# Performance work log

Hardware: AMD Instinct MI355X
Metric: run time of the kernel (lower is better)

Reference implementation:

```python
import jax, jax.numpy as jnp
import numpy as np

G = 512            # voxel grid extent per axis
B = 2              # batches
N_PER_BATCH = 20000
EPS = 1e-5
SLOPE = 0.01       # LeakyReLU default negative_slope
OFFS = [(dx, dy, dz) for dx in (-1, 0, 1) for dy in (-1, 0, 1) for dz in (-1, 0, 1)]


def _keys(coords, stride):
    # coords: [N,4] int32 (batch,x,y,z), multiples of stride -> unique int32 key
    Gs = G // stride
    c = coords[:, 1:] // stride
    return ((coords[:, 0] * Gs + c[:, 0]) * Gs + c[:, 1]) * Gs + c[:, 2]


def _sorted_keys(in_coords, in_stride):
    keys = _keys(in_coords, in_stride)
    perm = jnp.argsort(keys)
    return keys[perm], perm


def _query(ks, perm, out_coords, off, in_stride):
    # hash-free kernel-map lookup: binary search of neighbor key in sorted keys
    q = out_coords[:, 1:] + jnp.array(off, jnp.int32) * in_stride
    valid = jnp.all((q >= 0) & (q < G), axis=1)
    qc = jnp.clip(q, 0, G - 1) // in_stride
    Gs = G // in_stride
    qk = ((out_coords[:, 0] * Gs + qc[:, 0]) * Gs + qc[:, 1]) * Gs + qc[:, 2]
    pos = jnp.clip(jnp.searchsorted(ks, qk), 0, ks.shape[0] - 1)
    hit = valid & (ks[pos] == qk)
    return jnp.where(hit, perm[pos], 0), hit


def sparse_conv(feats, in_coords, out_coords, W, in_stride):
    # gather-GEMM-scatter sparse conv, kernel 3^3, W: [27, Cin, Cout]
    ks, perm = _sorted_keys(in_coords, in_stride)
    out = jnp.zeros((out_coords.shape[0], W.shape[-1]), feats.dtype)
    for k, off in enumerate(OFFS):
        idx, hit = _query(ks, perm, out_coords, off, in_stride)
        f = jnp.where(hit[:, None], feats[idx], jnp.zeros((), feats.dtype))
        out = out + f @ W[k]
    return out


def sparse_maxpool(feats, in_coords, out_coords, in_stride):
    ks, perm = _sorted_keys(in_coords, in_stride)
    NEG = jnp.asarray(-3.0e38, feats.dtype)
    out = jnp.full((out_coords.shape[0], feats.shape[1]), NEG, feats.dtype)
    for off in OFFS:
        idx, hit = _query(ks, perm, out_coords, off, in_stride)
        out = jnp.maximum(out, jnp.where(hit[:, None], feats[idx], NEG))
    return out


def slice_to_field(level_feats, level_coords, field_coords, stride):
    # TensorField.slice: map coarse sparse features back to every field point
    ks, perm = _sorted_keys(level_coords, stride)
    qk = _keys(field_coords, stride)
    pos = jnp.clip(jnp.searchsorted(ks, qk), 0, ks.shape[0] - 1)
    return level_feats[perm[pos]]


def bn_lrelu(x, gamma, beta):
    # MinkowskiBatchNorm (training-mode batch stats) + LeakyReLU
    mu = x.mean(0)
    var = ((x - mu) ** 2).mean(0)
    y = (x - mu) * jax.lax.rsqrt(var + EPS) * gamma + beta
    return jnp.where(y >= 0, y, SLOPE * y)


def setup_inputs() -> dict:
    rng = np.random.default_rng(0)
    coords_np = []
    for b in range(B):
        lin = np.unique(rng.integers(0, G ** 3, size=2 * N_PER_BATCH, dtype=np.int64))
        rng.shuffle(lin)
        lin = lin[:N_PER_BATCH]
        x, r = lin // (G * G), lin % (G * G)
        coords_np.append(np.stack([np.full(N_PER_BATCH, b, np.int64), x, r // G, r % G], 1))
    coords_np = np.concatenate(coords_np, 0)

    def level(s):
        q = coords_np.copy()
        q[:, 1:] = (q[:, 1:] // s) * s
        key = ((q[:, 0] * G + q[:, 1]) * G + q[:, 2]) * G + q[:, 3]
        uk = np.unique(key)
        b, r = uk // G ** 3, uk % G ** 3
        return np.stack([b, r // (G * G), (r // G) % G, r % G], 1).astype(np.int32)

    levels = {('c%d' % s): jnp.asarray(level(s)) for s in (2, 4, 8, 16, 32, 64, 128)}
    ks = jax.random.split(jax.random.key(0), 9)

    def conv_w(k, cin, cout):
        return jax.random.normal(k, (27, cin, cout), jnp.float32) * np.float32(np.sqrt(2.0 / (27 * cin)))

    inp = dict(
        feats=jax.random.normal(ks[0], (coords_np.shape[0], 1), jnp.float32),
        coords=jnp.asarray(coords_np.astype(np.int32)),
        w_mlp=jax.random.normal(ks[1], (1, 32), jnp.float32),
        gm=jnp.ones(32, jnp.float32), bm=jnp.zeros(32, jnp.float32),
        W1=conv_w(ks[2], 32, 48), g1=jnp.ones(48, jnp.float32), b1=jnp.zeros(48, jnp.float32),
        W2=conv_w(ks[3], 48, 64), g2=jnp.ones(64, jnp.float32), b2=jnp.zeros(64, jnp.float32),
        W3=conv_w(ks[4], 64, 96), g3=jnp.ones(96, jnp.float32), b3=jnp.zeros(96, jnp.float32),
        W4=conv_w(ks[5], 96, 128), g4=jnp.ones(128, jnp.float32), b4=jnp.zeros(128, jnp.float32),
        W5a=conv_w(ks[6], 336, 256), g5a=jnp.ones(256, jnp.float32), b5a=jnp.zeros(256, jnp.float32),
        W5b=conv_w(ks[7], 256, 512), g5b=jnp.ones(512, jnp.float32), b5b=jnp.zeros(512, jnp.float32),
        W5c=conv_w(ks[8], 512, 1024), g5c=jnp.ones(1024, jnp.float32), b5c=jnp.zeros(1024, jnp.float32),
    )
    inp.update(levels)
    return inp


def reference(feats, coords, c2, c4, c8, c16, c32, c64, c128, w_mlp, gm, bm,
              W1, g1, b1, W2, g2, b2, W3, g3, b3, W4, g4, b4,
              W5a, g5a, b5a, W5b, g5b, b5b, W5c, g5c, b5c):
    # mlp1 on the tensor field (coords are unique, so field == sparse tensor)
    x = bn_lrelu(feats @ w_mlp, gm, bm)                            # [N,32]
    y = bn_lrelu(sparse_conv(x, coords, coords, W1, 1), g1, b1)    # stride 1, 48
    y1 = sparse_maxpool(y, coords, c2, 1)                          # stride 2
    y = bn_lrelu(sparse_conv(y1, c2, c4, W2, 2), g2, b2)           # stride 4, 64
    y2 = sparse_maxpool(y, c4, c8, 4)                              # stride 8
    y = bn_lrelu(sparse_conv(y2, c8, c16, W3, 8), g3, b3)          # stride 16, 96
    y3 = sparse_maxpool(y, c16, c32, 16)                           # stride 32
    y = bn_lrelu(sparse_conv(y3, c32, c64, W4, 32), g4, b4)        # stride 64, 128
    y4 = sparse_maxpool(y, c64, c128, 64)                          # stride 128
    x1 = slice_to_field(y1, c2, coords, 2)
    x2 = slice_to_field(y2, c8, coords, 8)
    x3 = slice_to_field(y3, c32, coords, 32)
    x4 = slice_to_field(y4, c128, coords, 128)
    xc = jnp.concatenate([x1, x2, x3, x4], axis=1)                 # [N,336]
    y = bn_lrelu(sparse_conv(xc, coords, c2, W5a, 1), g5a, b5a)    # stride 2, 256
    y = bn_lrelu(sparse_conv(y, c2, c4, W5b, 2), g5b, b5b)         # stride 4, 512
    y = bn_lrelu(sparse_conv(y, c4, c8, W5c, 4), g5c, b5c)         # stride 8, 1024
    return y
```

## Files before the change

kernel.cpp:

```cpp
#include <hip/hip_runtime.h>
#include <cstdint>
#include <cstddef>

#define GDIM 512

typedef __attribute__((ext_vector_type(8))) short short8;
typedef __attribute__((ext_vector_type(4))) float f32x4;
typedef __attribute__((ext_vector_type(4))) unsigned short ushort4v;

__device__ __forceinline__ short f2bf(float f) {
  unsigned u = __float_as_uint(f);
  u = u + 0x7fffu + ((u >> 16) & 1u);
  return (short)(u >> 16);
}

__device__ __forceinline__ int hash_lookup(int key, const int* __restrict__ keys,
                                           const int* __restrict__ vals, unsigned capmask) {
  unsigned slot = ((unsigned)key * 2654435761u) & capmask;
  while (true) {
    int kk = keys[slot];
    if (kk == key) return vals[slot];
    if (kk == -1) return -1;
    slot = (slot + 1) & capmask;
  }
}

__global__ void k_build_table(const int* __restrict__ coords, int n, int sh, int Gs,
                              int* __restrict__ keys, int* __restrict__ vals, unsigned capmask) {
  int i = blockIdx.x * blockDim.x + threadIdx.x;
  if (i >= n) return;
  int b = coords[4 * i];
  int key = ((b * Gs + (coords[4 * i + 1] >> sh)) * Gs + (coords[4 * i + 2] >> sh)) * Gs +
            (coords[4 * i + 3] >> sh);
  unsigned slot = ((unsigned)key * 2654435761u) & capmask;
  while (true) {
    int prev = atomicCAS(&keys[slot], -1, key);
    if (prev == -1) { vals[slot] = i; return; }
    slot = (slot + 1) & capmask;
  }
}

__global__ void k_query_idx_t(const int* __restrict__ oc, int m, int sh, int Gs,
                              const int* __restrict__ keys, const int* __restrict__ vals,
                              unsigned capmask, int* __restrict__ idxT) {
  int k = blockIdx.y;
  int o = blockIdx.x * blockDim.x + threadIdx.x;
  if (o >= m) return;
  int stride = 1 << sh;
  int dx = k / 9 - 1, dy = (k / 3) % 3 - 1, dz = k % 3 - 1;
  int4 c = *(const int4*)(oc + 4 * o);
  int qx = c.y + dx * stride;
  int qy = c.z + dy * stride;
  int qz = c.w + dz * stride;
  int res = -1;
  if ((unsigned)qx < GDIM && (unsigned)qy < GDIM && (unsigned)qz < GDIM) {
    int key = ((c.x * Gs + (qx >> sh)) * Gs + (qy >> sh)) * Gs + (qz >> sh);
    res = hash_lookup(key, keys, vals, capmask);
  }
  idxT[(size_t)k * m + o] = res;
}

__global__ void k_make_pairs(const int* __restrict__ idxT, int m,
                             int* __restrict__ po_o, int* __restrict__ pi_o,
                             int* __restrict__ po_r, int* __restrict__ pi_r,
                             int* __restrict__ cnts, int mcap) {
  int o = blockIdx.x * blockDim.x + threadIdx.x;
  bool act = o < m;
  int lane = threadIdx.x & 63;
  bool owned = false;
  for (int k = 0; k < 27; ++k) {
    int i = act ? idxT[(size_t)k * m + o] : -1;
    bool hit = i >= 0;
    bool isown = hit && !owned;
    if (isown) owned = true;
    bool isrest = hit && !isown;
    unsigned long long bo = __ballot(isown);
    if (bo) {
      int ldr = __ffsll((unsigned long long)bo) - 1;
      int base = 0;
      if (lane == ldr) base = atomicAdd(&cnts[k], __popcll(bo));
      base = __shfl(base, ldr);
      if (isown) {
        int p = base + __popcll(bo & ((1ull << lane) - 1ull));
        po_o[k * mcap + p] = o;
        pi_o[k * mcap + p] = i;
      }
    }
    unsigned long long br = __ballot(isrest);
    if (br) {
      int ldr = __ffsll((unsigned long long)br) - 1;
      int base = 0;
      if (lane == ldr) base = atomicAdd(&cnts[27 + k], __popcll(br));
      base = __shfl(base, ldr);
      if (isrest) {
        int p = base + __popcll(br & ((1ull << lane) - 1ull));
        po_r[k * mcap + p] = o;
        pi_r[k * mcap + p] = i;
      }
    }
  }
}

__global__ void k_plan(const int* __restrict__ cnts, int* __restrict__ plan) {
  if (threadIdx.x == 0) {
    int acc = 0;
    for (int k = 0; k < 27; ++k) { plan[k] = acc; acc += (cnts[k] + 63) >> 6; }
    plan[27] = acc;
    acc = 0;
    for (int k = 0; k < 27; ++k) { plan[28 + k] = acc; acc += (cnts[27 + k] + 63) >> 6; }
    plan[55] = acc;
  }
}

template<bool OWNER>
__global__ __launch_bounds__(256) void k_conv_mfma(
    const unsigned short* __restrict__ Fb,
    const short* __restrict__ Wt,
    float* __restrict__ out,
    const int* __restrict__ plo, const int* __restrict__ pli,
    const int* __restrict__ counts, const int* __restrict__ plan,
    int cin, int cin_pad, int cout, int mcap) {
  __shared__ int pshared[28];
  __shared__ short Alds[64 * 136];
  __shared__ short Blds[2][128 * 40];
  __shared__ int rows_out[64];
  __shared__ int rows_in[64];

  int tid = threadIdx.x;
  if (tid < 28) pshared[tid] = plan[tid];
  __syncthreads();
  int NB = pshared[27];

  int n0 = blockIdx.y << 7;
  int wave = tid >> 6, lane = tid & 63;
  int wm = (wave & 1) * 32, wn = (wave >> 1) * 64;
  int lm = lane & 15, quad = lane >> 4;
  int bn0 = (tid) >> 2, bk0 = (tid & 3) << 3;
  int bn1 = (tid + 256) >> 2, bk1 = ((tid + 256) & 3) << 3;

  for (int v = blockIdx.x; v < NB; v += gridDim.x) {
    int k = 0;
    #pragma unroll
    for (int kk = 1; kk < 27; ++kk) k += (v >= pshared[kk]);
    int cnt = counts[k];
    int p0 = (v - pshared[k]) << 6;
    int np = min(64, cnt - p0);

    __syncthreads();
    if (tid < 64) {
      rows_out[tid] = (tid < np) ? plo[k * mcap + p0 + tid] : -1;
      rows_in [tid] = (tid < np) ? pli[k * mcap + p0 + tid] : -1;
    }
    const short* Wk = Wt + (size_t)k * cout * cin;
    f32x4 acc[2][4] = {};

    for (int ks = 0; ks < cin_pad; ks += 128) {
      int kslab = min(128, cin_pad - ks);
      int aStride = kslab + 8;
      __syncthreads();
      int clog = kslab == 128 ? 4 : (kslab == 64 ? 3 : 2);
      for (int u = tid; u < (64 << clog); u += 256) {
        int r = u >> clog;
        int kc = (u - (r << clog)) << 3;
        int gk = ks + kc;
        int irow = rows_in[r];
        short8 v8 = {0, 0, 0, 0, 0, 0, 0, 0};
        if (irow >= 0 && gk < cin)
          v8 = *(const short8*)((const short*)Fb + (size_t)irow * cin + gk);
        *(short8*)(Alds + r * aStride + kc) = v8;
      }
      int nsl = kslab >> 5;
      short8 br0 = {0, 0, 0, 0, 0, 0, 0, 0}, br1 = br0;
      {
        int gn = n0 + bn0, gk = ks + bk0;
        if (gn < cout && gk < cin) br0 = *(const short8*)(Wk + (size_t)gn * cin + gk);
        gn = n0 + bn1; gk = ks + bk1;
        if (gn < cout && gk < cin) br1 = *(const short8*)(Wk + (size_t)gn * cin + gk);
      }
      for (int j = 0; j < nsl; ++j) {
        __syncthreads();
        *(short8*)(&Blds[j & 1][bn0 * 40 + bk0]) = br0;
        *(short8*)(&Blds[j & 1][bn1 * 40 + bk1]) = br1;
        if (j + 1 < nsl) {
          int gkbase = ks + (j + 1) * 32;
          short8 z = {0, 0, 0, 0, 0, 0, 0, 0};
          br0 = z; br1 = z;
          int gn = n0 + bn0, gk = gkbase + bk0;
          if (gn < cout && gk < cin) br0 = *(const short8*)(Wk + (size_t)gn * cin + gk);
          gn = n0 + bn1; gk = gkbase + bk1;
          if (gn < cout && gk < cin) br1 = *(const short8*)(Wk + (size_t)gn * cin + gk);
        }
        __syncthreads();
        int ka = j * 32 + quad * 8;
        short8 a0 = *(const short8*)(Alds + (wm + lm) * aStride + ka);
        short8 a1 = *(const short8*)(Alds + (wm + 16 + lm) * aStride + ka);
        #pragma unroll
        for (int nt = 0; nt < 4; ++nt) {
          short8 b = *(const short8*)(&Blds[j & 1][(wn + nt * 16 + lm) * 40 + quad * 8]);
          acc[0][nt] = __builtin_amdgcn_mfma_f32_16x16x32_bf16(a0, b, acc[0][nt], 0, 0, 0);
          acc[1][nt] = __builtin_amdgcn_mfma_f32_16x16x32_bf16(a1, b, acc[1][nt], 0, 0, 0);
        }
      }
    }
    #pragma unroll
    for (int mt = 0; mt < 2; ++mt)
      #pragma unroll
      for (int nt = 0; nt < 4; ++nt)
        #pragma unroll
        for (int r = 0; r < 4; ++r) {
          int row = wm + mt * 16 + quad * 4 + r;
          int col = n0 + wn + nt * 16 + lm;
          if (row < np && col < cout) {
            if (OWNER)
              out[(size_t)rows_out[row] * cout + col] = acc[mt][nt][r];
            else
              atomicAdd(&out[(size_t)rows_out[row] * cout + col], acc[mt][nt][r]);
          }
        }
  }
}

__global__ void k_convert_w(const float* __restrict__ W, short* __restrict__ Wt,
                            int cin, int cout) {
  __shared__ float tile[32][33];
  int k = blockIdx.z;
  int n0 = blockIdx.x * 32, c0 = blockIdx.y * 32;
  int tx = threadIdx.x & 31, ty = threadIdx.x >> 5;
  const float* Wk = W + (size_t)k * cin * cout;
  for (int i = ty; i < 32; i += 8) {
    int c = c0 + i, n = n0 + tx;
    tile[i][tx] = (c < cin && n < cout) ? Wk[(size_t)c * cout + n] : 0.f;
  }
  __syncthreads();
  short* Wtk = Wt + (size_t)k * cout * cin;
  for (int i = ty; i < 32; i += 8) {
    int n = n0 + i, c = c0 + tx;
    if (n < cout && c < cin) Wtk[(size_t)n * cin + c] = f2bf(tile[tx][i]);
  }
}

__global__ void k_query_idx(const int* __restrict__ oc, int m, int sh, int Gs,
                            const int* __restrict__ keys, const int* __restrict__ vals,
                            unsigned capmask, int* __restrict__ idx) {
  int t = blockIdx.x * blockDim.x + threadIdx.x;
  if (t >= m * 27) return;
  int o = t / 27, k = t - o * 27;
  int stride = 1 << sh;
  int dx = k / 9 - 1, dy = (k / 3) % 3 - 1, dz = k % 3 - 1;
  int b  = oc[4 * o];
  int qx = oc[4 * o + 1] + dx * stride;
  int qy = oc[4 * o + 2] + dy * stride;
  int qz = oc[4 * o + 3] + dz * stride;
  int res = -1;
  if ((unsigned)qx < GDIM && (unsigned)qy < GDIM && (unsigned)qz < GDIM) {
    int key = ((b * Gs + (qx >> sh)) * Gs + (qy >> sh)) * Gs + (qz >> sh);
    res = hash_lookup(key, keys, vals, capmask);
  }
  idx[t] = res;
}

__global__ void k_maxpool_bn(const float* __restrict__ F, unsigned short* __restrict__ out,
                             const int* __restrict__ idx, int m, int C,
                             const float* __restrict__ ab) {
  long long t = (long long)blockIdx.x * blockDim.x + threadIdx.x;
  if (t >= (long long)m * C) return;
  int o = (int)(t / C), c = (int)(t - (long long)o * C);
  float a = ab[c], b = ab[C + c];
  float best = -3e38f;
  #pragma unroll 1
  for (int k = 0; k < 27; ++k) {
    int i = idx[o * 27 + k];
    if (i >= 0) {
      float y = a * F[(size_t)i * C + c] + b;
      y = fmaxf(y, 0.01f * y);
      best = fmaxf(best, y);
    }
  }
  out[t] = (unsigned short)f2bf(best);
}

__global__ void k_slice_idx(const int* __restrict__ coords, int n, int sh, int Gs,
                            const int* __restrict__ keys, const int* __restrict__ vals,
                            unsigned capmask, int* __restrict__ sidx) {
  int i = blockIdx.x * blockDim.x + threadIdx.x;
  if (i >= n) return;
  int b = coords[4 * i];
  int key = ((b * Gs + (coords[4 * i + 1] >> sh)) * Gs + (coords[4 * i + 2] >> sh)) * Gs +
            (coords[4 * i + 3] >> sh);
  int v = hash_lookup(key, keys, vals, capmask);
  sidx[i] = (v < 0) ? 0 : v;
}

__global__ void k_gather_cols16(const unsigned short* __restrict__ src, int C,
                                const int* __restrict__ sidx,
                                unsigned short* __restrict__ dst, int dstC, int colOff, int n) {
  long long t = (long long)blockIdx.x * blockDim.x + threadIdx.x;
  if (t >= (long long)n * C) return;
  int o = (int)(t / C), c = (int)(t - (long long)o * C);
  dst[(size_t)o * dstC + colOff + c] = src[(size_t)sidx[o] * C + c];
}

__global__ void k_mlp(const float* __restrict__ feats, const float* __restrict__ w,
                      float* __restrict__ x, int n) {
  int t = blockIdx.x * blockDim.x + threadIdx.x;
  if (t >= n * 32) return;
  x[t] = feats[t >> 5] * w[t & 31];
}

__global__ void k_bn_stats(const float* __restrict__ x, int m, int C,
                           float* __restrict__ sums) {
  __shared__ float ls[2][256];
  int tid = threadIdx.x;
  int RL = (C >= 256) ? 1 : (256 / C);
  int c, rl;
  bool active;
  if (C >= 256) { c = blockIdx.y * 256 + tid; rl = 0; active = true; }
  else { c = tid % C; rl = tid / C; active = (tid < RL * C); }
  float s = 0.f, s2 = 0.f;
  if (active) {
    int step = gridDim.x * RL;
    for (int r = blockIdx.x * RL + rl; r < m; r += step) {
      float v = x[(size_t)r * C + c];
      s += v; s2 += v * v;
    }
  }
  if (RL == 1) {
    atomicAdd(&sums[c], s);
    atomicAdd(&sums[C + c], s2);
  } else {
    ls[0][tid] = s; ls[1][tid] = s2;
    __syncthreads();
    if (tid < C) {
      for (int j = 1; j < RL; ++j) { s += ls[0][c + j * C]; s2 += ls[1][c + j * C]; }
      atomicAdd(&sums[c], s);
      atomicAdd(&sums[C + c], s2);
    }
  }
}

__global__ void k_bn_finalize(const float* __restrict__ sums, const float* __restrict__ gamma,
                              const float* __restrict__ beta, int C, float inv_m,
                              float* __restrict__ ab) {
  for (int c = threadIdx.x; c < C; c += 256) {
    float mu  = sums[c] * inv_m;
    float var = sums[C + c] * inv_m - mu * mu;
    float a = rsqrtf(var + 1e-5f) * gamma[c];
    ab[c] = a;
    ab[C + c] = beta[c] - mu * a;
  }
}

__global__ void k_bn_bf16(const float* __restrict__ x, unsigned short* __restrict__ xb,
                          long long total4, int C, const float* __restrict__ ab) {
  long long t = (long long)blockIdx.x * blockDim.x + threadIdx.x;
  if (t >= total4) return;
  long long e = t * 4;
  int c = (int)(e % C);
  float4 v = *(const float4*)(x + e);
  ushort4v o;
  float y0 = ab[c] * v.x + ab[C + c];         o.x = (unsigned short)f2bf(fmaxf(y0, 0.01f * y0));
  float y1 = ab[c + 1] * v.y + ab[C + c + 1]; o.y = (unsigned short)f2bf(fmaxf(y1, 0.01f * y1));
  float y2 = ab[c + 2] * v.z + ab[C + c + 2]; o.z = (unsigned short)f2bf(fmaxf(y2, 0.01f * y2));
  float y3 = ab[c + 3] * v.w + ab[C + c + 3]; o.w = (unsigned short)f2bf(fmaxf(y3, 0.01f * y3));
  *(ushort4v*)(xb + e) = o;
}

__global__ void k_bn_apply(float* __restrict__ x, long long total4, int C,
                           const float* __restrict__ ab) {
  long long t = (long long)blockIdx.x * blockDim.x + threadIdx.x;
  if (t >= total4) return;
  long long e = t * 4;
  int c = (int)(e % C);
  float4 v = *(const float4*)(x + e);
  float y0 = ab[c] * v.x + ab[C + c];         v.x = fmaxf(y0, 0.01f * y0);
  float y1 = ab[c + 1] * v.y + ab[C + c + 1]; v.y = fmaxf(y1, 0.01f * y1);
  float y2 = ab[c + 2] * v.z + ab[C + c + 2]; v.z = fmaxf(y2, 0.01f * y2);
  float y3 = ab[c + 3] * v.w + ab[C + c + 3]; v.w = fmaxf(y3, 0.01f * y3);
  *(float4*)(x + e) = v;
}

static inline int cdiv(int a, int b) { return (a + b - 1) / b; }

extern "C" void kernel_launch(void* const* d_in, const int* in_sizes, int n_in,
                              void* d_out, int out_size, void* d_ws, size_t ws_size,
                              hipStream_t stream) {
  (void)n_in; (void)out_size; (void)ws_size;
  const float* feats  = (const float*)d_in[0];
  const int*   coords = (const int*)d_in[1];
  const float* w_mlp = (const float*)d_in[2];
  const float* gm  = (const float*)d_in[3];  const float* bm  = (const float*)d_in[4];
  const float* W1  = (const float*)d_in[5];  const float* g1  = (const float*)d_in[6];  const float* b1  = (const float*)d_in[7];
  const float* W2  = (const float*)d_in[8];  const float* g2  = (const float*)d_in[9];  const float* b2  = (const float*)d_in[10];
  const float* W3  = (const float*)d_in[11]; const float* g3  = (const float*)d_in[12]; const float* b3  = (const float*)d_in[13];
  const float* W4  = (const float*)d_in[14]; const float* g4  = (const float*)d_in[15]; const float* b4  = (const float*)d_in[16];
  const float* W5a = (const float*)d_in[17]; const float* g5a = (const float*)d_in[18]; const float* b5a = (const float*)d_in[19];
  const float* W5b = (const float*)d_in[20]; const float* g5b = (const float*)d_in[21]; const float* b5b = (const float*)d_in[22];
  const float* W5c = (const float*)d_in[23]; const float* g5c = (const float*)d_in[24]; const float* b5c = (const float*)d_in[25];
  const int*   lvl[7];
  for (int i = 0; i < 7; ++i) lvl[i] = (const int*)d_in[26 + i];

  const int N = in_sizes[0];
  int nl[7];
  for (int i = 0; i < 7; ++i) nl[i] = in_sizes[26 + i] / 4;
  const int n2 = nl[0], n4 = nl[1], n8 = nl[2], n16 = nl[3], n32 = nl[4], n64 = nl[5], n128 = nl[6];

  char* ws = (char*)d_ws;
  size_t off = 0;
  auto alloc = [&](size_t bytes) -> char* {
    off = (off + 255) & ~(size_t)255;
    char* p = ws + off;
    off += bytes;
    return p;
  };

  struct Tab { int* keys; int* vals; unsigned mask; int sh; int Gs; int n; const int* src; };
  Tab tab[8];
  const int* tsrc[8] = {coords, lvl[0], lvl[1], lvl[2], lvl[3], lvl[4], lvl[5], lvl[6]};
  int tn[8] = {N, n2, n4, n8, n16, n32, n64, n128};
  for (int i = 0; i < 8; ++i) {
    int cap = 64;
    while (cap < 2 * tn[i]) cap <<= 1;
    tab[i].keys = (int*)alloc((size_t)cap * 4);
    tab[i].vals = (int*)alloc((size_t)cap * 4);
    tab[i].mask = (unsigned)(cap - 1);
    tab[i].sh = i;
    tab[i].Gs = GDIM >> i;
    tab[i].n = tn[i];
    tab[i].src = tsrc[i];
  }

  int* pout   = (int*)alloc((size_t)27 * N * 4);
  int* pin    = (int*)alloc((size_t)27 * N * 4);
  int* pout_r = (int*)alloc((size_t)27 * N * 4);
  int* pin_r  = (int*)alloc((size_t)27 * N * 4);
  int* counts = (int*)alloc(256);
  int* plan   = (int*)alloc(256);
  int* idxbuf = (int*)alloc((size_t)27 * N * 4);
  int* sidx[4];
  for (int i = 0; i < 4; ++i) sidx[i] = (int*)alloc((size_t)N * 4);
  float* bnsum = (float*)alloc(2 * 1024 * 4);
  float* abuf  = (float*)alloc(2 * 1024 * 4);

  auto mxz = [](size_t a, size_t b) { return a > b ? a : b; };
  size_t szA = mxz(mxz((size_t)N * 32, (size_t)n4 * 64), (size_t)n64 * 128) * 4;
  size_t szB = mxz(mxz((size_t)N * 48, (size_t)n16 * 96), (size_t)n2 * 256) * 4;
  float* RA = (float*)alloc(szA);
  float* RB = (float*)alloc(szB);
  float* RG = (float*)alloc((size_t)n4 * 512 * 4);
  unsigned short* xb  = (unsigned short*)alloc((size_t)N * 32 * 2);
  unsigned short* y1b = (unsigned short*)alloc((size_t)n2 * 48 * 2);
  unsigned short* y2b = (unsigned short*)alloc((size_t)n8 * 64 * 2);
  unsigned short* y3b = (unsigned short*)alloc((size_t)n32 * 96 * 2);
  unsigned short* y4b = (unsigned short*)alloc((size_t)n128 * 128 * 2);
  unsigned short* xcb = (unsigned short*)alloc((size_t)N * 336 * 2);
  unsigned short* t5bb = (unsigned short*)alloc((size_t)n4 * 512 * 2);
  short* Wt1  = (short*)alloc((size_t)27 * 32 * 48 * 2);
  short* Wt2  = (short*)alloc((size_t)27 * 48 * 64 * 2);
  short* Wt3  = (short*)alloc((size_t)27 * 64 * 96 * 2);
  short* Wt4  = (short*)alloc((size_t)27 * 96 * 128 * 2);
  short* Wt5a = (short*)alloc((size_t)27 * 336 * 256 * 2);
  short* Wt5b = (short*)alloc((size_t)27 * 256 * 512 * 2);
  short* Wt5c = (short*)alloc((size_t)27 * 512 * 1024 * 2);

  for (int i = 0; i < 8; ++i)
    hipMemsetAsync(tab[i].keys, 0xFF, (size_t)(tab[i].mask + 1) * 4, stream);
  for (int i = 0; i < 8; ++i)
    k_build_table<<<cdiv(tab[i].n, 256), 256, 0, stream>>>(
        tab[i].src, tab[i].n, tab[i].sh, tab[i].Gs, tab[i].keys, tab[i].vals, tab[i].mask);

  auto convW = [&](const float* W, short* Wt, int cin, int cout) {
    dim3 g(cdiv(cout, 32), cdiv(cin, 32), 27);
    k_convert_w<<<g, 256, 0, stream>>>(W, Wt, cin, cout);
  };
  convW(W1, Wt1, 32, 48);     convW(W2, Wt2, 48, 64);
  convW(W3, Wt3, 64, 96);     convW(W4, Wt4, 96, 128);
  convW(W5a, Wt5a, 336, 256); convW(W5b, Wt5b, 256, 512);
  convW(W5c, Wt5c, 512, 1024);

  auto conv = [&](const unsigned short* Fb, const short* Wt, const int* oc, int m,
                  const Tab& t, int cin, int cout, float* out) {
    hipMemsetAsync(counts, 0, 54 * 4, stream);
    dim3 gq(cdiv(m, 256), 27);
    k_query_idx_t<<<gq, 256, 0, stream>>>(oc, m, t.sh, t.Gs, t.keys, t.vals, t.mask, idxbuf);
    k_make_pairs<<<cdiv(m, 256), 256, 0, stream>>>(idxbuf, m, pout, pin, pout_r, pin_r,
                                                   counts, N);
    k_plan<<<1, 64, 0, stream>>>(counts, plan);
    int cin_pad = cin <= 32 ? 32 : (cin <= 64 ? 64 : ((cin + 127) & ~127));
    int nT = cdiv(cout, 128);
    int G = cdiv(m, 64) + 27;
    if (G > 2048) G = 2048;
    dim3 gridc(G, nT);
    k_conv_mfma<true><<<gridc, 256, 0, stream>>>(Fb, Wt, out, pout, pin, counts, plan,
                                                 cin, cin_pad, cout, N);
    k_conv_mfma<false><<<gridc, 256, 0, stream>>>(Fb, Wt, out, pout_r, pin_r, counts + 27,
                                                  plan + 28, cin, cin_pad, cout, N);
  };
  auto stats = [&](const float* x, int m, int C, const float* gamma, const float* beta) {
    hipMemsetAsync(bnsum, 0, (size_t)2 * C * 4, stream);
    int CG = (C >= 256) ? (C / 256) : 1;
    int RL = (C >= 256) ? 1 : (256 / C);
    int NS = (C >= 256) ? 512 : 256;
    int maxNS = cdiv(m, RL);
    if (NS > maxNS) NS = maxNS < 1 ? 1 : maxNS;
    dim3 g(NS, CG);
    k_bn_stats<<<g, 256, 0, stream>>>(x, m, C, bnsum);
    k_bn_finalize<<<1, 256, 0, stream>>>(bnsum, gamma, beta, C, 1.0f / (float)m, abuf);
  };
  auto pool = [&](const float* F, const int* oc, int m, const Tab& t, int C,
                  unsigned short* out) {
    k_query_idx<<<cdiv(m * 27, 256), 256, 0, stream>>>(
        oc, m, t.sh, t.Gs, t.keys, t.vals, t.mask, idxbuf);
    long long total = (long long)m * C;
    k_maxpool_bn<<<(int)((total + 255) / 256), 256, 0, stream>>>(F, out, idxbuf, m, C, abuf);
  };
  auto cvt = [&](const float* src, unsigned short* dst, long long total, int C) {
    long long t4 = total / 4;
    k_bn_bf16<<<(int)((t4 + 255) / 256), 256, 0, stream>>>(src, dst, t4, C, abuf);
  };

  float* x = RA;
  k_mlp<<<cdiv(N * 32, 256), 256, 0, stream>>>(feats, w_mlp, x, N);
  stats(x, N, 32, gm, bm);
  cvt(x, xb, (long long)N * 32, 32);

  float* t1 = RB;
  conv(xb, Wt1, coords, N, tab[0], 32, 48, t1);
  stats(t1, N, 48, g1, b1);
  pool(t1, lvl[0], n2, tab[0], 48, y1b);

  float* t2 = RA;
  conv(y1b, Wt2, lvl[1], n4, tab[1], 48, 64, t2);
  stats(t2, n4, 64, g2, b2);
  pool(t2, lvl[2], n8, tab[2], 64, y2b);

  float* t3 = RB;
  conv(y2b, Wt3, lvl[3], n16, tab[3], 64, 96, t3);
  stats(t3, n16, 96, g3, b3);
  pool(t3, lvl[4], n32, tab[4], 96, y3b);

  float* t4 = RA;
  conv(y3b, Wt4, lvl[5], n64, tab[5], 96, 128, t4);
  stats(t4, n64, 128, g4, b4);
  pool(t4, lvl[6], n128, tab[6], 128, y4b);

  k_slice_idx<<<cdiv(N, 256), 256, 0, stream>>>(coords, N, tab[1].sh, tab[1].Gs,
                                                tab[1].keys, tab[1].vals, tab[1].mask, sidx[0]);
  k_slice_idx<<<cdiv(N, 256), 256, 0, stream>>>(coords, N, tab[3].sh, tab[3].Gs,
                                                tab[3].keys, tab[3].vals, tab[3].mask, sidx[1]);
  k_slice_idx<<<cdiv(N, 256), 256, 0, stream>>>(coords, N, tab[5].sh, tab[5].Gs,
                                                tab[5].keys, tab[5].vals, tab[5].mask, sidx[2]);
  k_slice_idx<<<cdiv(N, 256), 256, 0, stream>>>(coords, N, tab[7].sh, tab[7].Gs,
                                                tab[7].keys, tab[7].vals, tab[7].mask, sidx[3]);
  k_gather_cols16<<<(int)(((long long)N * 48 + 255) / 256), 256, 0, stream>>>(y1b, 48, sidx[0], xcb, 336, 0, N);
  k_gather_cols16<<<(int)(((long long)N * 64 + 255) / 256), 256, 0, stream>>>(y2b, 64, sidx[1], xcb, 336, 48, N);
  k_gather_cols16<<<(int)(((long long)N * 96 + 255) / 256), 256, 0, stream>>>(y3b, 96, sidx[2], xcb, 336, 112, N);
  k_gather_cols16<<<(int)(((long long)N * 128 + 255) / 256), 256, 0, stream>>>(y4b, 128, sidx[3], xcb, 336, 208, N);

  float* t5a = RB;
  conv(xcb, Wt5a, lvl[0], n2, tab[0], 336, 256, t5a);
  stats(t5a, n2, 256, g5a, b5a);
  unsigned short* t5ab = xcb;
  cvt(t5a, t5ab, (long long)n2 * 256, 256);

  float* t5b = RG;
  conv(t5ab, Wt5b, lvl[1], n4, tab[1], 256, 512, t5b);
  stats(t5b, n4, 512, g5b, b5b);
  cvt(t5b, t5bb, (long long)n4 * 512, 512);

  float* outp = (float*)d_out;
  conv(t5bb, Wt5c, lvl[2], n8, tab[2], 512, 1024, outp);
  stats(outp, n8, 1024, g5c, b5c);
  long long total4 = (long long)n8 * 1024 / 4;
  k_bn_apply<<<(int)((total4 + 255) / 256), 256, 0, stream>>>(outp, total4, 1024, abuf);
}
```

Before: 1.861 ms.

## Enlarge conv GEMM M tile to 128 rows and restructure K loop

Each block of the gather-GEMM conv kernel now covers 128 pair rows instead of 64. Each wave holds a 4x4 grid of MFMA accumulators, so every B fragment loaded from LDS feeds twice as many MFMAs. The K loop becomes a single 32-wide step loop that refills the A tile every 64 channels, with cin padded only to a multiple of 32. The grid is transposed so N tiles share blockIdx.x and neighbouring blocks reuse the same gathered rows. Costs are more accumulator registers (lower occupancy), fewer blocks for small layers, and more padding waste on partial 128-row tiles.

```diff
diff --git a/kernel.cpp b/kernel.cpp
--- a/kernel.cpp
+++ b/kernel.cpp
@@ -104,10 +104,10 @@
 __global__ void k_plan(const int* __restrict__ cnts, int* __restrict__ plan) {
   if (threadIdx.x == 0) {
     int acc = 0;
-    for (int k = 0; k < 27; ++k) { plan[k] = acc; acc += (cnts[k] + 63) >> 6; }
+    for (int k = 0; k < 27; ++k) { plan[k] = acc; acc += (cnts[k] + 127) >> 7; }
     plan[27] = acc;
     acc = 0;
-    for (int k = 0; k < 27; ++k) { plan[28 + k] = acc; acc += (cnts[27 + k] + 63) >> 6; }
+    for (int k = 0; k < 27; ++k) { plan[28 + k] = acc; acc += (cnts[27 + k] + 127) >> 7; }
     plan[55] = acc;
   }
 }
@@ -121,89 +121,92 @@
     const int* __restrict__ counts, const int* __restrict__ plan,
     int cin, int cin_pad, int cout, int mcap) {
   __shared__ int pshared[28];
-  __shared__ short Alds[64 * 136];
+  __shared__ short Alds[128 * 72];
   __shared__ short Blds[2][128 * 40];
-  __shared__ int rows_out[64];
-  __shared__ int rows_in[64];
+  __shared__ int rows_out[128];
+  __shared__ int rows_in[128];
 
   int tid = threadIdx.x;
   if (tid < 28) pshared[tid] = plan[tid];
   __syncthreads();
   int NB = pshared[27];
 
-  int n0 = blockIdx.y << 7;
+  int n0 = blockIdx.x << 7;
   int wave = tid >> 6, lane = tid & 63;
-  int wm = (wave & 1) * 32, wn = (wave >> 1) * 64;
+  int wm = (wave & 1) * 64, wn = (wave >> 1) * 64;
   int lm = lane & 15, quad = lane >> 4;
-  int bn0 = (tid) >> 2, bk0 = (tid & 3) << 3;
+  int bn0 = tid >> 2, bk0 = (tid & 3) << 3;
   int bn1 = (tid + 256) >> 2, bk1 = ((tid + 256) & 3) << 3;
-
-  for (int v = blockIdx.x; v < NB; v += gridDim.x) {
+  int S = cin_pad >> 5;
+
+  for (int v = blockIdx.y; v < NB; v += gridDim.y) {
     int k = 0;
     #pragma unroll
     for (int kk = 1; kk < 27; ++kk) k += (v >= pshared[kk]);
     int cnt = counts[k];
-    int p0 = (v - pshared[k]) << 6;
-    int np = min(64, cnt - p0);
+    int p0 = (v - pshared[k]) << 7;
+    int np = min(128, cnt - p0);
 
     __syncthreads();
-    if (tid < 64) {
+    if (tid < 128) {
       rows_out[tid] = (tid < np) ? plo[k * mcap + p0 + tid] : -1;
       rows_in [tid] = (tid < np) ? pli[k * mcap + p0 + tid] : -1;
     }
     const short* Wk = Wt + (size_t)k * cout * cin;
-    f32x4 acc[2][4] = {};
-
-    for (int ks = 0; ks < cin_pad; ks += 128) {
-      int kslab = min(128, cin_pad - ks);
-      int aStride = kslab + 8;
+    f32x4 acc[4][4] = {};
+
+    short8 br0 = {0, 0, 0, 0, 0, 0, 0, 0}, br1 = br0;
+    {
+      int gn = n0 + bn0;
+      if (gn < cout && bk0 < cin) br0 = *(const short8*)(Wk + (size_t)gn * cin + bk0);
+      gn = n0 + bn1;
+      if (gn < cout && bk1 < cin) br1 = *(const short8*)(Wk + (size_t)gn * cin + bk1);
+    }
+    for (int s = 0; s < S; ++s) {
+      int ks = s << 5;
       __syncthreads();
-      int clog = kslab == 128 ? 4 : (kslab == 64 ? 3 : 2);
-      for (int u = tid; u < (64 << clog); u += 256) {
-        int r = u >> clog;
-        int kc = (u - (r << clog)) << 3;
-        int gk = ks + kc;
-        int irow = rows_in[r];
-        short8 v8 = {0, 0, 0, 0, 0, 0, 0, 0};
-        if (irow >= 0 && gk < cin)
-          v8 = *(const short8*)((const short*)Fb + (size_t)irow * cin + gk);
-        *(short8*)(Alds + r * aStride + kc) = v8;
+      if ((s & 1) == 0) {
+        int kslab = min(64, cin_pad - ks);
+        int clog = (kslab == 64) ? 3 : 2;
+        for (int u = tid; u < (128 << clog); u += 256) {
+          int r = u >> clog;
+          int kc = (u - (r << clog)) << 3;
+          int gk = ks + kc;
+          int irow = rows_in[r];
+          short8 v8 = {0, 0, 0, 0, 0, 0, 0, 0};
+          if (irow >= 0 && gk < cin)
+            v8 = *(const short8*)((const short*)Fb + (size_t)irow * cin + gk);
+          *(short8*)(Alds + r * 72 + kc) = v8;
+        }
       }
-      int nsl = kslab >> 5;
-      short8 br0 = {0, 0, 0, 0, 0, 0, 0, 0}, br1 = br0;
-      {
-        int gn = n0 + bn0, gk = ks + bk0;
+      *(short8*)(&Blds[s & 1][bn0 * 40 + bk0]) = br0;
+      *(short8*)(&Blds[s & 1][bn1 * 40 + bk1]) = br1;
+      if (s + 1 < S) {
+        int gkb = (s + 1) << 5;
+        short8 z = {0, 0, 0, 0, 0, 0, 0, 0};
+        br0 = z; br1 = z;
+        int gn = n0 + bn0, gk = gkb + bk0;
         if (gn < cout && gk < cin) br0 = *(const short8*)(Wk + (size_t)gn * cin + gk);
-        gn = n0 + bn1; gk = ks + bk1;
+        gn = n0 + bn1; gk = gkb + bk1;
         if (gn < cout && gk < cin) br1 = *(const short8*)(Wk + (size_t)gn * cin + gk);
       }
-      for (int j = 0; j < nsl; ++j) {
-        __syncthreads();
-        *(short8*)(&Blds[j & 1][bn0 * 40 + bk0]) = br0;
-        *(short8*)(&Blds[j & 1][bn1 * 40 + bk1]) = br1;
-        if (j + 1 < nsl) {
-          int gkbase = ks + (j + 1) * 32;
-          short8 z = {0, 0, 0, 0, 0, 0, 0, 0};
-          br0 = z; br1 = z;
-          int gn = n0 + bn0, gk = gkbase + bk0;
-          if (gn < cout && gk < cin) br0 = *(const short8*)(Wk + (size_t)gn * cin + gk);
-          gn = n0 + bn1; gk = gkbase + bk1;
-          if (gn < cout && gk < cin) br1 = *(const short8*)(Wk + (size_t)gn * cin + gk);
-        }
-        __syncthreads();
-        int ka = j * 32 + quad * 8;
-        short8 a0 = *(const short8*)(Alds + (wm + lm) * aStride + ka);
-        short8 a1 = *(const short8*)(Alds + (wm + 16 + lm) * aStride + ka);
+      __syncthreads();
+      int ka = ((s & 1) << 5) + quad * 8;
+      short8 a[4], b[4];
+      #pragma unroll
+      for (int mt = 0; mt < 4; ++mt)
+        a[mt] = *(const short8*)(Alds + (wm + mt * 16 + lm) * 72 + ka);
+      #pragma unroll
+      for (int nt = 0; nt < 4; ++nt)
+        b[nt] = *(const short8*)(&Blds[s & 1][(wn + nt * 16 + lm) * 40 + quad * 8]);
+      #pragma unroll
+      for (int mt = 0; mt < 4; ++mt)
         #pragma unroll
-        for (int nt = 0; nt < 4; ++nt) {
-          short8 b = *(const short8*)(&Blds[j & 1][(wn + nt * 16 + lm) * 40 + quad * 8]);
-          acc[0][nt] = __builtin_amdgcn_mfma_f32_16x16x32_bf16(a0, b, acc[0][nt], 0, 0, 0);
-          acc[1][nt] = __builtin_amdgcn_mfma_f32_16x16x32_bf16(a1, b, acc[1][nt], 0, 0, 0);
-        }
-      }
+        for (int nt = 0; nt < 4; ++nt)
+          acc[mt][nt] = __builtin_amdgcn_mfma_f32_16x16x32_bf16(a[mt], b[nt], acc[mt][nt], 0, 0, 0);
     }
     #pragma unroll
-    for (int mt = 0; mt < 2; ++mt)
+    for (int mt = 0; mt < 4; ++mt)
       #pragma unroll
       for (int nt = 0; nt < 4; ++nt)
         #pragma unroll
@@ -485,11 +488,11 @@
     k_make_pairs<<<cdiv(m, 256), 256, 0, stream>>>(idxbuf, m, pout, pin, pout_r, pin_r,
                                                    counts, N);
     k_plan<<<1, 64, 0, stream>>>(counts, plan);
-    int cin_pad = cin <= 32 ? 32 : (cin <= 64 ? 64 : ((cin + 127) & ~127));
+    int cin_pad = (cin + 31) & ~31;
     int nT = cdiv(cout, 128);
-    int G = cdiv(m, 64) + 27;
-    if (G > 2048) G = 2048;
-    dim3 gridc(G, nT);
+    int GY = cdiv(m, 128) + 27;
+    if (GY > 2048) GY = 2048;
+    dim3 gridc(nT, GY);
     k_conv_mfma<true><<<gridc, 256, 0, stream>>>(Fb, Wt, out, pout, pin, counts, plan,
                                                  cin, cin_pad, cout, N);
     k_conv_mfma<false><<<gridc, 256, 0, stream>>>(Fb, Wt, out, pout_r, pin_r, counts + 27,
```

Measured after the change: 1.820 ms. 1.02x faster.
